# Performance work log

Measured on AMD Instinct MI355X. Metric: run time of the kernel, lower is better.

Reference implementation:

```python
import jax, jax.numpy as jnp
import numpy as np

B, C, H, W = 32, 2, 512, 512


def setup_inputs() -> dict:
    key = jax.random.key(0)
    k1, k2 = jax.random.split(key)
    inp = jax.random.normal(k1, (B, C, H, W), dtype=jnp.float32)
    tgt = jax.random.normal(k2, (B, C, H, W), dtype=jnp.float32)
    return {"input": inp, "target": tgt}


def reference(input, target):
    b, c, h, w = input.shape
    dt = input.dtype
    # coordinate maps: (index+1)/size, kept fused via broadcasting
    x_map = jnp.arange(1, w + 1, dtype=dt) / w          # [W]
    y_map = (jnp.arange(1, h + 1, dtype=dt) / h)[:, None]  # [H,1]
    # per-(sample, channel) softmax over flattened heatmap (DSNT)
    sm = jax.nn.softmax(input.reshape(b, c, h * w), axis=-1).reshape(b, c, h, w)
    # soft-argmax coords in normalized range, then *size -> pixel coords
    pred_x = jnp.sum(sm * x_map, axis=(-2, -1)) * w     # [B,C] pixel
    pred_y = jnp.sum(sm * y_map, axis=(-2, -1)) * h     # [B,C] pixel
    # hard argmax for ground truth; ((idx % W + 1)/W)*W == idx % W + 1
    idx = jnp.argmax(target.reshape(b, c, h * w), axis=-1)  # [B,C]
    true_x = (idx % w + 1).astype(dt)                   # [B,C] pixel
    true_y = (idx // w + 1).astype(dt)                  # [B,C] pixel
    # per-point euclidean pixel distance
    ed = jnp.sqrt((true_x - pred_x) ** 2 + (true_y - pred_y) ** 2)  # [B,C]
    s_i = jnp.sum(ed[:, 0])  # channel 0: inferior
    s_s = jnp.sum(ed[:, 1])  # channel 1: superior
    # diameter (distance between the two points) difference, abs via sqrt(sq)
    pred_pts = jnp.stack([pred_x, pred_y], axis=-1)  # [B,C,2]
    true_pts = jnp.stack([true_x, true_y], axis=-1)  # [B,C,2]
    vp = pred_pts[:, 0] - pred_pts[:, 1]             # [B,2]
    vt = true_pts[:, 0] - true_pts[:, 1]             # [B,2]
    pred_dist = jnp.sqrt(jnp.sum(vp ** 2, axis=-1))
    true_dist = jnp.sqrt(jnp.sum(vt ** 2, axis=-1))
    s_diam = jnp.sum(jnp.sqrt((pred_dist - true_dist) ** 2))
    bn = jnp.asarray(b, dt)
    # coordinate lists (pixel coord - 1 as index), ordered batch-major then channel
    pred_coords = (pred_pts - 1.0).reshape(b * c, 2)
    true_coords = (true_pts - 1.0).reshape(b * c, 2)
    return (s_i / bn, s_s / bn, (s_i + s_s) / bn, s_diam / bn,
            pred_coords, true_coords)
```

## Files before the change

kernel.cpp:

```cpp
#include <hip/hip_runtime.h>
#include <math.h>

#define BATCH 32
#define CHANS 2
#define HH 512
#define WW 512
#define BC (BATCH * CHANS)
#define HMAP (HH * WW)
#define SPLITS 64
#define CHUNK (HMAP / SPLITS)
#define THREADS 256

typedef float vf4 __attribute__((ext_vector_type(4)));

__global__ __launch_bounds__(THREADS)
void dsnt_partial(const float* __restrict__ inp, const float* __restrict__ tgt,
                  float* __restrict__ ps, float* __restrict__ psx,
                  float* __restrict__ psy, float* __restrict__ pmv,
                  int* __restrict__ pix) {
    const int split = blockIdx.x;
    const int bc    = blockIdx.y;
    const long base = (long)bc * HMAP + (long)split * CHUNK;
    const vf4* in4 = (const vf4*)(inp + base);
    const vf4* tg4 = (const vf4*)(tgt + base);
    const int t = threadIdx.x;

    vf4 x0 = __builtin_nontemporal_load(&in4[t]);
    vf4 x1 = __builtin_nontemporal_load(&in4[t + 1 * THREADS]);
    vf4 x2 = __builtin_nontemporal_load(&in4[t + 2 * THREADS]);
    vf4 x3 = __builtin_nontemporal_load(&in4[t + 3 * THREADS]);
    vf4 g0 = __builtin_nontemporal_load(&tg4[t]);
    vf4 g1 = __builtin_nontemporal_load(&tg4[t + 1 * THREADS]);
    vf4 g2 = __builtin_nontemporal_load(&tg4[t + 2 * THREADS]);
    vf4 g3 = __builtin_nontemporal_load(&tg4[t + 3 * THREADS]);
    asm volatile("" ::: "memory");

    float s = 0.f, sx = 0.f, sy = 0.f;
    float bm = -INFINITY;
    int   bi = 0;

#define CONSUME(X, G, J)                                                    \
    {                                                                       \
        const int p = split * CHUNK + (t + (J) * THREADS) * 4;              \
        const float wy = (float)((p >> 9) + 1);                             \
        const float wx = (float)((p & 511) + 1);                            \
        const float e0 = __expf(X.x), e1 = __expf(X.y);                     \
        const float e2 = __expf(X.z), e3 = __expf(X.w);                     \
        const float es = (e0 + e1) + (e2 + e3);                             \
        s  += es;                                                           \
        sx += es * wx + (e1 + 2.f * e2 + 3.f * e3);                         \
        sy += es * wy;                                                      \
        if (G.x > bm) { bm = G.x; bi = p;     }                             \
        if (G.y > bm) { bm = G.y; bi = p + 1; }                             \
        if (G.z > bm) { bm = G.z; bi = p + 2; }                             \
        if (G.w > bm) { bm = G.w; bi = p + 3; }                             \
    }

    CONSUME(x0, g0, 0)
    CONSUME(x1, g1, 1)
    CONSUME(x2, g2, 2)
    CONSUME(x3, g3, 3)
#undef CONSUME

    const int lane = t & 63;
    const int wave = t >> 6;
    #pragma unroll
    for (int off = 32; off > 0; off >>= 1) {
        s  += __shfl_down(s,  off, 64);
        sx += __shfl_down(sx, off, 64);
        sy += __shfl_down(sy, off, 64);
        const float om = __shfl_down(bm, off, 64);
        const int   oi = __shfl_down(bi, off, 64);
        if (om > bm || (om == bm && oi < bi)) { bm = om; bi = oi; }
    }

    __shared__ float shs[4], shsx[4], shsy[4], shm[4];
    __shared__ int   shi[4];
    if (lane == 0) { shs[wave] = s; shsx[wave] = sx; shsy[wave] = sy;
                     shm[wave] = bm; shi[wave] = bi; }
    __syncthreads();
    if (t == 0) {
        float S = shs[0], SX = shsx[0], SY = shsy[0], M = shm[0];
        int   I = shi[0];
        #pragma unroll
        for (int w = 1; w < 4; ++w) {
            S += shs[w]; SX += shsx[w]; SY += shsy[w];
            if (shm[w] > M || (shm[w] == M && shi[w] < I)) { M = shm[w]; I = shi[w]; }
        }
        const int o = split * BC + bc;
        ps[o] = S; psx[o] = SX; psy[o] = SY; pmv[o] = M; pix[o] = I;
    }
}

__global__ __launch_bounds__(256)
void dsnt_final(const float* __restrict__ ps, const float* __restrict__ psx,
                const float* __restrict__ psy, const float* __restrict__ pmv,
                const int* __restrict__ pix, float* __restrict__ out) {
    const int t    = threadIdx.x;
    const int lane = t & 63;
    const int wv   = t >> 6;

    float S = 0.f, SX = 0.f, SY = 0.f, M = -INFINITY;
    int I = 0;
    #pragma unroll
    for (int k = 0; k < SPLITS / 4; ++k) {
        const int o = (wv * (SPLITS / 4) + k) * BC + lane;
        S += ps[o]; SX += psx[o]; SY += psy[o];
        const float v = pmv[o];
        const int  ix = pix[o];
        if (v > M || (v == M && ix < I)) { M = v; I = ix; }
    }

    __shared__ float lS[4][64], lSX[4][64], lSY[4][64], lM[4][64];
    __shared__ int   lI[4][64];
    lS[wv][lane] = S; lSX[wv][lane] = SX; lSY[wv][lane] = SY;
    lM[wv][lane] = M; lI[wv][lane] = I;
    __syncthreads();
    if (wv != 0) return;

    #pragma unroll
    for (int w = 1; w < 4; ++w) {
        S += lS[w][lane]; SX += lSX[w][lane]; SY += lSY[w][lane];
        const float v = lM[w][lane];
        const int  ix = lI[w][lane];
        if (v > M || (v == M && ix < I)) { M = v; I = ix; }
    }

    const float px = SX / S;
    const float py = SY / S;
    const float tx = (float)((I & 511) + 1);
    const float ty = (float)((I >> 9) + 1);
    const float dx = tx - px, dy = ty - py;
    const float ed = sqrtf(dx * dx + dy * dy);

    out[4 + lane * 2 + 0]   = px - 1.f;
    out[4 + lane * 2 + 1]   = py - 1.f;
    out[132 + lane * 2 + 0] = tx - 1.f;
    out[133 + lane * 2]     = ty - 1.f;

    const float opx = __shfl_xor(px, 1, 64);
    const float opy = __shfl_xor(py, 1, 64);
    const float otx = __shfl_xor(tx, 1, 64);
    const float oty = __shfl_xor(ty, 1, 64);
    float dterm = 0.f;
    if ((lane & 1) == 0) {
        const float vpx = px - opx, vpy = py - opy;
        const float vtx = tx - otx, vty = ty - oty;
        const float pd = sqrtf(vpx * vpx + vpy * vpy);
        const float td = sqrtf(vtx * vtx + vty * vty);
        dterm = fabsf(pd - td);
    }
    float e0 = ((lane & 1) == 0) ? ed : 0.f;
    float e1 = ((lane & 1) == 1) ? ed : 0.f;
    #pragma unroll
    for (int off = 32; off > 0; off >>= 1) {
        e0    += __shfl_down(e0, off, 64);
        e1    += __shfl_down(e1, off, 64);
        dterm += __shfl_down(dterm, off, 64);
    }
    if (lane == 0) {
        const float inv = 1.0f / (float)BATCH;
        out[0] = e0 * inv;
        out[1] = e1 * inv;
        out[2] = (e0 + e1) * inv;
        out[3] = dterm * inv;
    }
}

extern "C" void kernel_launch(void* const* d_in, const int* in_sizes, int n_in,
                              void* d_out, int out_size, void* d_ws, size_t ws_size,
                              hipStream_t stream) {
    const float* inp = (const float*)d_in[0];
    const float* tgt = (const float*)d_in[1];
    float* out = (float*)d_out;

    float* ps  = (float*)d_ws;
    float* psx = ps  + BC * SPLITS;
    float* psy = psx + BC * SPLITS;
    float* pmv = psy + BC * SPLITS;
    int*   pix = (int*)(pmv + BC * SPLITS);

    dim3 grid(SPLITS, BC);
    dsnt_partial<<<grid, THREADS, 0, stream>>>(inp, tgt, ps, psx, psy, pmv, pix);
    dsnt_final<<<1, 256, 0, stream>>>(ps, psx, psy, pmv, pix, out);
}
```

Measured before the change: 142.6 us.

## Fuse final reduction via last-block atomic counter and double-buffer larger chunks

Merges the two-kernel scheme into one kernel: each block writes its partials, increments an atomic counter, and the last block to finish performs the final reduction and writes the outputs. The split count drops from 64 to 16, so each block handles four times more data, and the loads are double-buffered in two register sets so the next batch is in flight while the current one is consumed. This removes a second kernel launch and cuts the number of partials. In exchange it adds a memset on the stream, threadfence and atomic overhead, and a grid of 1024 blocks, which may give less latency hiding per CU.

```diff
diff --git a/kernel.cpp b/kernel.cpp
--- a/kernel.cpp
+++ b/kernel.cpp
@@ -7,41 +7,52 @@
 #define WW 512
 #define BC (BATCH * CHANS)
 #define HMAP (HH * WW)
-#define SPLITS 64
+#define SPLITS 16
 #define CHUNK (HMAP / SPLITS)
 #define THREADS 256
+#define NBLOCKS (SPLITS * BC)
 
 typedef float vf4 __attribute__((ext_vector_type(4)));
 
 __global__ __launch_bounds__(THREADS)
-void dsnt_partial(const float* __restrict__ inp, const float* __restrict__ tgt,
-                  float* __restrict__ ps, float* __restrict__ psx,
-                  float* __restrict__ psy, float* __restrict__ pmv,
-                  int* __restrict__ pix) {
+void dsnt_fused(const float* __restrict__ inp, const float* __restrict__ tgt,
+                float* __restrict__ ps, float* __restrict__ psx,
+                float* __restrict__ psy, float* __restrict__ pmv,
+                int* __restrict__ pix, int* __restrict__ counter,
+                float* __restrict__ out) {
     const int split = blockIdx.x;
     const int bc    = blockIdx.y;
     const long base = (long)bc * HMAP + (long)split * CHUNK;
     const vf4* in4 = (const vf4*)(inp + base);
     const vf4* tg4 = (const vf4*)(tgt + base);
-    const int t = threadIdx.x;
-
-    vf4 x0 = __builtin_nontemporal_load(&in4[t]);
-    vf4 x1 = __builtin_nontemporal_load(&in4[t + 1 * THREADS]);
-    vf4 x2 = __builtin_nontemporal_load(&in4[t + 2 * THREADS]);
-    vf4 x3 = __builtin_nontemporal_load(&in4[t + 3 * THREADS]);
-    vf4 g0 = __builtin_nontemporal_load(&tg4[t]);
-    vf4 g1 = __builtin_nontemporal_load(&tg4[t + 1 * THREADS]);
-    vf4 g2 = __builtin_nontemporal_load(&tg4[t + 2 * THREADS]);
-    vf4 g3 = __builtin_nontemporal_load(&tg4[t + 3 * THREADS]);
-    asm volatile("" ::: "memory");
+    const int t    = threadIdx.x;
+    const int lane = t & 63;
+    const int wave = t >> 6;
 
     float s = 0.f, sx = 0.f, sy = 0.f;
     float bm = -INFINITY;
     int   bi = 0;
 
-#define CONSUME(X, G, J)                                                    \
+    vf4 xa0, xa1, xa2, xa3, ga0, ga1, ga2, ga3;
+    vf4 xb0, xb1, xb2, xb3, gb0, gb1, gb2, gb3;
+
+#define LOAD(X0, X1, X2, X3, G0, G1, G2, G3, K)                             \
     {                                                                       \
-        const int p = split * CHUNK + (t + (J) * THREADS) * 4;              \
+        const int o = (K) * 1024 + t;                                       \
+        X0 = __builtin_nontemporal_load(&in4[o]);                           \
+        X1 = __builtin_nontemporal_load(&in4[o + 256]);                     \
+        X2 = __builtin_nontemporal_load(&in4[o + 512]);                     \
+        X3 = __builtin_nontemporal_load(&in4[o + 768]);                     \
+        G0 = __builtin_nontemporal_load(&tg4[o]);                           \
+        G1 = __builtin_nontemporal_load(&tg4[o + 256]);                     \
+        G2 = __builtin_nontemporal_load(&tg4[o + 512]);                     \
+        G3 = __builtin_nontemporal_load(&tg4[o + 768]);                     \
+        asm volatile("" ::: "memory");                                      \
+    }
+
+#define CONS1(X, G, K, J)                                                   \
+    {                                                                       \
+        const int p = split * CHUNK + ((K) * 1024 + (J) * 256 + t) * 4;     \
         const float wy = (float)((p >> 9) + 1);                             \
         const float wx = (float)((p & 511) + 1);                            \
         const float e0 = __expf(X.x), e1 = __expf(X.y);                     \
@@ -55,15 +66,21 @@
         if (G.z > bm) { bm = G.z; bi = p + 2; }                             \
         if (G.w > bm) { bm = G.w; bi = p + 3; }                             \
     }
-
-    CONSUME(x0, g0, 0)
-    CONSUME(x1, g1, 1)
-    CONSUME(x2, g2, 2)
-    CONSUME(x3, g3, 3)
-#undef CONSUME
-
-    const int lane = t & 63;
-    const int wave = t >> 6;
+#define CONSA(K) CONS1(xa0, ga0, K, 0) CONS1(xa1, ga1, K, 1) \
+                 CONS1(xa2, ga2, K, 2) CONS1(xa3, ga3, K, 3)
+#define CONSB(K) CONS1(xb0, gb0, K, 0) CONS1(xb1, gb1, K, 1) \
+                 CONS1(xb2, gb2, K, 2) CONS1(xb3, gb3, K, 3)
+
+    LOAD(xa0, xa1, xa2, xa3, ga0, ga1, ga2, ga3, 0)
+    LOAD(xb0, xb1, xb2, xb3, gb0, gb1, gb2, gb3, 1) CONSA(0)
+    LOAD(xa0, xa1, xa2, xa3, ga0, ga1, ga2, ga3, 2) CONSB(1)
+    LOAD(xb0, xb1, xb2, xb3, gb0, gb1, gb2, gb3, 3) CONSA(2)
+    CONSB(3)
+#undef LOAD
+#undef CONS1
+#undef CONSA
+#undef CONSB
+
     #pragma unroll
     for (int off = 32; off > 0; off >>= 1) {
         s  += __shfl_down(s,  off, 64);
@@ -76,6 +93,7 @@
 
     __shared__ float shs[4], shsx[4], shsy[4], shm[4];
     __shared__ int   shi[4];
+    __shared__ int   isLast;
     if (lane == 0) { shs[wave] = s; shsx[wave] = sx; shsy[wave] = sy;
                      shm[wave] = bm; shi[wave] = bi; }
     __syncthreads();
@@ -89,25 +107,25 @@
         }
         const int o = split * BC + bc;
         ps[o] = S; psx[o] = SX; psy[o] = SY; pmv[o] = M; pix[o] = I;
-    }
-}
-
-__global__ __launch_bounds__(256)
-void dsnt_final(const float* __restrict__ ps, const float* __restrict__ psx,
-                const float* __restrict__ psy, const float* __restrict__ pmv,
-                const int* __restrict__ pix, float* __restrict__ out) {
-    const int t    = threadIdx.x;
-    const int lane = t & 63;
-    const int wv   = t >> 6;
-
+        __threadfence();
+        const int old = atomicAdd(counter, 1);
+        isLast = (old == NBLOCKS - 1) ? 1 : 0;
+    }
+    __syncthreads();
+    if (!isLast) return;
+    __threadfence();
+
+    const int wv = wave;
     float S = 0.f, SX = 0.f, SY = 0.f, M = -INFINITY;
     int I = 0;
     #pragma unroll
     for (int k = 0; k < SPLITS / 4; ++k) {
         const int o = (wv * (SPLITS / 4) + k) * BC + lane;
-        S += ps[o]; SX += psx[o]; SY += psy[o];
-        const float v = pmv[o];
-        const int  ix = pix[o];
+        S  += __builtin_nontemporal_load(&ps[o]);
+        SX += __builtin_nontemporal_load(&psx[o]);
+        SY += __builtin_nontemporal_load(&psy[o]);
+        const float v = __builtin_nontemporal_load(&pmv[o]);
+        const int  ix = __builtin_nontemporal_load(&pix[o]);
         if (v > M || (v == M && ix < I)) { M = v; I = ix; }
     }
 
@@ -175,12 +193,15 @@
     float* out = (float*)d_out;
 
     float* ps  = (float*)d_ws;
-    float* psx = ps  + BC * SPLITS;
-    float* psy = psx + BC * SPLITS;
-    float* pmv = psy + BC * SPLITS;
-    int*   pix = (int*)(pmv + BC * SPLITS);
+    float* psx = ps  + NBLOCKS;
+    float* psy = psx + NBLOCKS;
+    float* pmv = psy + NBLOCKS;
+    int*   pix = (int*)(pmv + NBLOCKS);
+    int*   cnt = pix + NBLOCKS;
+
+    hipMemsetAsync(cnt, 0, sizeof(int), stream);
 
     dim3 grid(SPLITS, BC);
-    dsnt_partial<<<grid, THREADS, 0, stream>>>(inp, tgt, ps, psx, psy, pmv, pix);
-    dsnt_final<<<1, 256, 0, stream>>>(ps, psx, psy, pmv, pix, out);
+    dsnt_fused<<<grid, THREADS, 0, stream>>>(inp, tgt, ps, psx, psy, pmv, pix,
+                                             cnt, out);
 }
```

New measurement: 188.8 us. 1.32x slower.
